# Optimization experiments

Hardware: AMD Instinct MI355X
Metric: run time of the kernel (lower is better)

## Reference

```python
import jax, jax.numpy as jnp
import numpy as np

B, C, M, H, W = 4, 12, 2, 320, 320
TOL = 1e-6
MAX_ITER = 10


def to_c(t):
    # [..., 2] real -> complex
    return jax.lax.complex(t[..., 0], t[..., 1])


def to_r(t):
    return jnp.stack([jnp.real(t), jnp.imag(t)], axis=-1)


def fft2c(x):
    return jnp.fft.fft2(x, axes=(-2, -1), norm='ortho')


def ifft2c(x):
    return jnp.fft.ifft2(x, axes=(-2, -1), norm='ortho')


def A_op(x, sm, mk):
    # x: [B,M,H,W] complex, sm: [B,C,M,H,W] complex, mk: [B,C,H,W] real
    coil_imgs = jnp.sum(x[:, None] * sm, axis=2)  # [B,C,H,W]
    return fft2c(coil_imgs) * mk


def AT_op(y, sm, mk):
    img = ifft2c(y * mk)  # [B,C,H,W]
    return jnp.sum(jnp.conj(sm) * img[:, :, None], axis=1)  # [B,M,H,W]


def cg_solve(x0, Mop, tol=TOL, max_iter=MAX_ITER):
    b = x0.shape[0]
    x0x0 = jnp.sum(jnp.abs(x0.reshape(b, -1)) ** 2, axis=-1)  # [B] real

    def body(carry, _):
        x, r, p, rr = carry
        active = jnp.min(rr / x0x0) > tol  # tol check, gated like the while-loop
        q = Mop(p)
        pq = jnp.sum((p * jnp.conj(q)).reshape(b, -1), axis=-1)  # complexDot(p, q)
        alpha = rr.astype(x0.dtype) / pq  # complex_div(rr, <p,q>)
        a = alpha[:, None, None, None]
        x_new = x + a * p
        r_new = r - a * q
        rr_new = jnp.sum(jnp.abs(r_new.reshape(b, -1)) ** 2, axis=-1)
        beta = (rr_new / rr)[:, None, None, None].astype(x0.dtype)
        p_new = r_new + beta * p
        new = (x_new, r_new, p_new, rr_new)
        carry = jax.tree.map(lambda n, o: jnp.where(active, n, o), new, carry)
        return carry, None

    rr0 = jnp.sum(jnp.abs(x0.reshape(b, -1)) ** 2, axis=-1)
    init = (jnp.zeros_like(x0), x0, x0, rr0)
    (x, _, _, _), _ = jax.lax.scan(body, init, None, length=max_iter)
    return x


def setup_inputs() -> dict:
    key = jax.random.key(0)
    k1, k2, k3, k4 = jax.random.split(key, 4)
    x = jax.random.normal(k1, (B, M, H, W, 2), dtype=jnp.float32)
    y = jax.random.normal(k2, (B, C, H, W, 2), dtype=jnp.float32)
    smaps = jax.random.normal(k3, (B, C, M, H, W, 2), dtype=jnp.float32) * 0.2
    mask = jax.random.randint(k4, (B, C, H, W, 1), 0, 2).astype(jnp.float32)
    lambda_a = jnp.full((1,), 0.05, dtype=jnp.float32)
    return {"x": x, "y": y, "smaps": smaps, "mask": mask, "lambda_a": lambda_a}


def reference(x, y, smaps, mask, lambda_a):
    z = to_c(x)          # [B,M,H,W]
    yc = to_c(y)         # [B,C,H,W]
    sm = to_c(smaps)     # [B,C,M,H,W]
    mk = mask[..., 0]    # [B,C,H,W]
    lam = lambda_a[0]

    x0 = lam * AT_op(yc, sm, mk) + z

    def Mop(p):
        return lam * AT_op(A_op(p, sm, mk), sm, mk) + p

    return to_r(cg_solve(x0, Mop))
```

## Files before the change

### kernel.cpp

```cpp
#include <hip/hip_runtime.h>
#include <math.h>

#define NB 4
#define NC 12
#define NM 2
#define NN 320
#define NHW (NN*NN)
#define NBC (NB*NC)
#define CG_TOL 1e-6f
#define NITER 10
#define PBLK 400
#define QBLK 320
#define CPG 3
#define NG  4
#define TROW 4
#define LSTR (NN + 2)

#define TWO_PI_F 6.28318530717958647692f

typedef float2 c32;

__device__ __forceinline__ c32 cmul(c32 a, c32 b){ return make_float2(a.x*b.x - a.y*b.y, a.x*b.y + a.y*b.x); }
__device__ __forceinline__ c32 cmulj(c32 a, c32 b){ return make_float2(a.x*b.x + a.y*b.y, a.x*b.y - a.y*b.x); }
__device__ __forceinline__ c32 cadd(c32 a, c32 b){ return make_float2(a.x+b.x, a.y+b.y); }
__device__ __forceinline__ c32 csub(c32 a, c32 b){ return make_float2(a.x-b.x, a.y-b.y); }
__device__ __forceinline__ c32 cscale(c32 a, float s){ return make_float2(a.x*s, a.y*s); }

template<bool CONJ>
__device__ __forceinline__ c32 twmul(c32 a, c32 t){
  return CONJ ? make_float2(a.x*t.x + a.y*t.y, a.y*t.x - a.x*t.y)
              : make_float2(a.x*t.x - a.y*t.y, a.y*t.x + a.x*t.y);
}

__device__ __forceinline__ float wave_reduce_f(float v) {
  #pragma unroll
  for (int off = 32; off >= 1; off >>= 1) v += __shfl_xor(v, off, 64);
  return v;
}
__device__ __forceinline__ c32 wave_reduce_c(c32 v) {
  #pragma unroll
  for (int off = 32; off >= 1; off >>= 1) {
    v.x += __shfl_xor(v.x, off, 64);
    v.y += __shfl_xor(v.y, off, 64);
  }
  return v;
}

__global__ __launch_bounds__(256)
void twiddle_init(c32* __restrict__ T320, c32* __restrict__ T64)
{
  const int t = threadIdx.x;
  {
    float s, c; sincosf(TWO_PI_F * (float)t / 320.f, &s, &c);
    T320[t] = make_float2(c, s);
  }
  if (t < 32) {
    float s, c; sincosf(TWO_PI_F * (float)t / 64.f, &s, &c);
    T64[t] = make_float2(c, s);
  }
}

template<bool FWD>
__device__ __forceinline__ void radix5(c32 V[5]) {
  constexpr float C1 = 0.30901699437494745f;
  constexpr float S1 = 0.9510565162951535f;
  constexpr float C2 = -0.8090169943749475f;
  constexpr float S2 = 0.5877852522924731f;
  constexpr float sg = FWD ? -1.f : 1.f;
  const c32 w1 = make_float2(C1,  sg*S1);
  const c32 w2 = make_float2(C2,  sg*S2);
  const c32 w3 = make_float2(C2, -sg*S2);
  const c32 w4 = make_float2(C1, -sg*S1);
  c32 v0=V[0], v1=V[1], v2=V[2], v3=V[3], v4=V[4];
  V[0] = cadd(cadd(v0, v1), cadd(cadd(v2, v3), v4));
  V[1] = cadd(v0, cadd(cadd(cmul(v1,w1), cmul(v2,w2)), cadd(cmul(v3,w3), cmul(v4,w4))));
  V[2] = cadd(v0, cadd(cadd(cmul(v1,w2), cmul(v2,w4)), cadd(cmul(v3,w1), cmul(v4,w3))));
  V[3] = cadd(v0, cadd(cadd(cmul(v1,w3), cmul(v2,w1)), cadd(cmul(v3,w4), cmul(v4,w2))));
  V[4] = cadd(v0, cadd(cadd(cmul(v1,w4), cmul(v2,w3)), cadd(cmul(v3,w2), cmul(v4,w1))));
}

template<bool FWD>
__device__ __forceinline__ void fft320_one(c32 A[5], const c32 ct[4], const c32 tw[6], int lane)
{
  radix5<FWD>(A);
  #pragma unroll
  for (int k = 1; k < 5; ++k) A[k] = twmul<FWD>(A[k], ct[k-1]);
  #pragma unroll
  for (int s = 0; s < 6; ++s) {
    const int m = 32 >> s;
    const c32 w = tw[s];
    const bool up = (lane & m) != 0;
    c32 o[5];
    #pragma unroll
    for (int k = 0; k < 5; ++k) { o[k].x = __shfl_xor(A[k].x, m, 64); o[k].y = __shfl_xor(A[k].y, m, 64); }
    #pragma unroll
    for (int k = 0; k < 5; ++k) {
      c32 lo = cadd(A[k], o[k]);
      c32 hi = twmul<FWD>(csub(o[k], A[k]), w);
      A[k] = up ? hi : lo;
    }
  }
}

__device__ __forceinline__ void ifft320_dit(c32 A[5], const c32 ct[4], const c32 tw[6], int lane)
{
  #pragma unroll
  for (int s = 5; s >= 0; --s) {
    const int m = 32 >> s;
    const c32 w = tw[s];
    const bool up = (lane & m) != 0;
    #pragma unroll
    for (int k = 0; k < 5; ++k) {
      c32 t = up ? twmul<false>(A[k], w) : A[k];
      c32 o; o.x = __shfl_xor(t.x, m, 64); o.y = __shfl_xor(t.y, m, 64);
      A[k] = up ? csub(o, t) : cadd(t, o);
    }
  }
  #pragma unroll
  for (int k = 1; k < 5; ++k) A[k] = twmul<false>(A[k], ct[k-1]);
  radix5<false>(A);
}

#define LOAD_TWIDDLES \
  c32 ct[4], tw[6]; \
  _Pragma("unroll") for (int k_ = 0; k_ < 4; ++k_) ct[k_] = T320[(k_ + 1) * lane]; \
  _Pragma("unroll") for (int s_ = 0; s_ < 6; ++s_) tw[s_] = T64[(lane & ((32 >> s_) - 1)) << s_];

__global__ __launch_bounds__(256)
void setup_mask_ifft(const c32* __restrict__ in, c32* __restrict__ out,
                     const float* __restrict__ mask,
                     const c32* __restrict__ T320, const c32* __restrict__ T64)
{
  __shared__ c32 tile[TROW][LSTR];
  const int tid = threadIdx.x, lane = tid & 63, wv = tid >> 6;
  const int by = blockIdx.y, b = by >> 2, g = by & 3;
  const int r0 = blockIdx.x * TROW;
  const int row = r0 + wv;
  LOAD_TWIDDLES
  const int rv6 = __brev((unsigned)lane) >> 26;
  for (int cc = 0; cc < CPG; ++cc) {
    const int bc = b*NC + g*CPG + cc;
    c32 A[5];
    #pragma unroll
    for (int j = 0; j < 5; ++j) {
      const size_t idx = ((size_t)bc * NN + row) * NN + lane + 64*j;
      A[j] = cscale(in[idx], mask[idx]);
    }
    fft320_one<false>(A, ct, tw, lane);
    __syncthreads();
    #pragma unroll
    for (int k = 0; k < 5; ++k) tile[wv][k + 5*rv6] = A[k];
    __syncthreads();
    #pragma unroll
    for (int it = 0; it < 5; ++it) {
      const int idx = it * 256 + tid, u = idx >> 2, d = idx & 3;
      out[((size_t)bc * NN + u) * NN + (r0 + d)] = tile[d][u];
    }
  }
}

__global__ __launch_bounds__(256)
void setup_init(const c32* __restrict__ bufin, const c32* __restrict__ smaps,
                c32* __restrict__ pacc,
                const c32* __restrict__ T320, const c32* __restrict__ T64)
{
  __shared__ c32 tile[TROW][LSTR];
  const int tid = threadIdx.x, lane = tid & 63, wv = tid >> 6;
  const int by = blockIdx.y, b = by >> 2, g = by & 3;
  const int r0 = blockIdx.x * TROW;
  const int w = r0 + wv;
  LOAD_TWIDDLES
  const int rv6 = __brev((unsigned)lane) >> 26;
  c32 acc0[5], acc1[5];
  #pragma unroll
  for (int it = 0; it < 5; ++it) { acc0[it] = make_float2(0.f,0.f); acc1[it] = make_float2(0.f,0.f); }

  for (int cc = 0; cc < CPG; ++cc) {
    const int c = g*CPG + cc;
    c32 A[5];
    #pragma unroll
    for (int j = 0; j < 5; ++j)
      A[j] = bufin[((size_t)(b*NC + c) * NN + w) * NN + lane + 64*j];
    fft320_one<false>(A, ct, tw, lane);
    __syncthreads();
    #pragma unroll
    for (int k = 0; k < 5; ++k) tile[wv][k + 5*rv6] = A[k];
    __syncthreads();
    #pragma unroll
    for (int it = 0; it < 5; ++it) {
      const int idx = it * 256 + tid, u = idx >> 2, d = idx & 3;
      c32 v = tile[d][u];
      c32 s0 = smaps[(size_t)((b*NC + c)*NM + 0) * NHW + (size_t)u * NN + (r0 + d)];
      c32 s1 = smaps[(size_t)((b*NC + c)*NM + 1) * NHW + (size_t)u * NN + (r0 + d)];
      acc0[it] = cadd(acc0[it], cmulj(s0, v));
      acc1[it] = cadd(acc1[it], cmulj(s1, v));
    }
  }
  #pragma unroll
  for (int it = 0; it < 5; ++it) {
    const int idx = it * 256 + tid, u = idx >> 2, d = idx & 3;
    const size_t hw = (size_t)u * NN + (r0 + d);
    pacc[(size_t)((g*NB + b)*NM + 0) * NHW + hw] = acc0[it];
    pacc[(size_t)((g*NB + b)*NM + 1) * NHW + hw] = acc1[it];
  }
}

__global__ __launch_bounds__(256)
void setup_fin(const c32* __restrict__ pacc, const c32* __restrict__ z,
               c32* __restrict__ x, c32* __restrict__ r, c32* __restrict__ p,
               const float* __restrict__ lam, float* __restrict__ part)
{
  const int b  = blockIdx.y;
  const int hw = blockIdx.x * 256 + threadIdx.x;
  const float l0 = lam[0] * (1.f / (float)NN);
  float accf = 0.f;
  #pragma unroll
  for (int m = 0; m < NM; ++m) {
    c32 a = make_float2(0.f, 0.f);
    #pragma unroll
    for (int g = 0; g < NG; ++g)
      a = cadd(a, pacc[(size_t)((g*NB + b)*NM + m) * NHW + hw]);
    const size_t im = (size_t)(b*NM + m) * NHW + hw;
    c32 x0v = cadd(cscale(a, l0), z[im]);
    x[im] = make_float2(0.f, 0.f);
    r[im] = x0v; p[im] = x0v;
    accf += x0v.x*x0v.x + x0v.y*x0v.y;
  }
  accf = wave_reduce_f(accf);
  __shared__ float sred[4];
  const int lane = threadIdx.x & 63, wv = threadIdx.x >> 6;
  if (lane == 0) sred[wv] = accf;
  __syncthreads();
  if (threadIdx.x == 0) part[b*PBLK + blockIdx.x] = sred[0]+sred[1]+sred[2]+sred[3];
}

__global__ __launch_bounds__(256)
void fft_comb_deep(c32* __restrict__ out, const c32* __restrict__ pin,
                   const c32* __restrict__ rres, c32* __restrict__ pout,
                   const c32* __restrict__ smaps,
                   float* __restrict__ rr, float* __restrict__ flags,
                   const float* __restrict__ part1, const int it,
                   const c32* __restrict__ T320, const c32* __restrict__ T64)
{
  __shared__ c32 tile[TROW][LSTR];
  __shared__ float sstat[NB];
  const int tid = threadIdx.x, lane = tid & 63, wv = tid >> 6;
  const int by = blockIdx.y, b = by >> 2, g = by & 3;
  const int r0 = blockIdx.x * TROW;
  const int row = r0 + wv;
  {
    float s = 0.f;
    for (int j = lane; j < PBLK; j += 64) s += part1[wv*PBLK + j];
    s = wave_reduce_f(s);
    if (lane == 0) sstat[wv] = s;
  }
  __syncthreads();
  float flag;
  if (it == 0) flag = 1.f;
  else {
    float mn = 1e30f;
    #pragma unroll
    for (int bb = 0; bb < NB; ++bb) mn = fminf(mn, sstat[bb] / rr[bb]);
    flag = (mn > CG_TOL) ? 1.f : 0.f;
  }
  if (tid < NB) rr[it*NB + tid] = sstat[tid];
  if (tid == 0) flags[it] = flag;
  if (it != 0 && flag == 0.f) return;
  const float beta = (it != 0) ? sstat[b] / rr[(it-1)*NB + b] : 0.f;

  LOAD_TWIDDLES
  const int rv6 = __brev((unsigned)lane) >> 26;
  const size_t m0 = (size_t)(b*NM + 0) * NHW, m1 = (size_t)(b*NM + 1) * NHW;
  c32 p0[5], p1[5];
  #pragma unroll
  for (int j = 0; j < 5; ++j) {
    const size_t h = (size_t)row * NN + lane + 64*j;
    c32 r0v = rres[m0 + h], r1v = rres[m1 + h];
    if (it != 0) {
      p0[j] = cadd(r0v, cscale(pin[m0 + h], beta));
      p1[j] = cadd(r1v, cscale(pin[m1 + h], beta));
      if (g == 0) { pout[m0 + h] = p0[j]; pout[m1 + h] = p1[j]; }
    } else { p0[j] = r0v; p1[j] = r1v; }
  }
  for (int cc = 0; cc < CPG; ++cc) {
    const int c = g * CPG + cc;
    const size_t s0o = (size_t)((b*NC + c)*NM + 0) * NHW, s1o = (size_t)((b*NC + c)*NM + 1) * NHW;
    c32 A[5];
    #pragma unroll
    for (int j = 0; j < 5; ++j) {
      const size_t h = (size_t)row * NN + lane + 64*j;
      A[j] = cadd(cmul(p0[j], smaps[s0o + h]), cmul(p1[j], smaps[s1o + h]));
    }
    fft320_one<true>(A, ct, tw, lane);
    __syncthreads();
    #pragma unroll
    for (int k = 0; k < 5; ++k) tile[wv][k + 5*rv6] = A[k];
    __syncthreads();
    #pragma unroll
    for (int itr = 0; itr < 5; ++itr) {
      const int idx = itr * 256 + tid, u = idx >> 2, d = idx & 3;
      out[(size_t)(b*NC + c) * NHW + (size_t)u * NN + (r0 + d)] = tile[d][u];
    }
  }
}

__global__ __launch_bounds__(256)
void fmi_deep(const c32* __restrict__ in, c32* __restrict__ out,
              const float* __restrict__ mask, const float* __restrict__ flag,
              const c32* __restrict__ T320, const c32* __restrict__ T64)
{
  if (flag[0] == 0.f) return;
  __shared__ c32 tile[TROW][LSTR];
  const int tid = threadIdx.x, lane = tid & 63, wv = tid >> 6;
  const int by = blockIdx.y, b = by >> 2, g = by & 3;
  const int r0 = blockIdx.x * TROW;
  const int row = r0 + wv;
  LOAD_TWIDDLES
  const int rv6 = __brev((unsigned)lane) >> 26;
  for (int cc = 0; cc < CPG; ++cc) {
    const int bc = b*NC + g*CPG + cc;
    c32 A[5];
    #pragma unroll
    for (int j = 0; j < 5; ++j)
      A[j] = in[((size_t)bc * NN + row) * NN + lane + 64*j];
    fft320_one<true>(A, ct, tw, lane);
    #pragma unroll
    for (int k = 0; k < 5; ++k) {
      const int kh = k + 5*rv6;
      A[k] = cscale(A[k], mask[(size_t)bc * NHW + (size_t)kh * NN + row]);
    }
    ifft320_dit(A, ct, tw, lane);
    __syncthreads();
    #pragma unroll
    for (int j = 0; j < 5; ++j) tile[wv][lane + 64*j] = A[j];
    __syncthreads();
    #pragma unroll
    for (int it = 0; it < 5; ++it) {
      const int idx = it * 256 + tid, u = idx >> 2, d = idx & 3;
      out[(size_t)bc * NHW + (size_t)u * NN + (r0 + d)] = tile[d][u];
    }
  }
}

__global__ __launch_bounds__(256)
void ifft_q(const c32* __restrict__ bufin, const c32* __restrict__ smaps,
            const c32* __restrict__ p, c32* __restrict__ q,
            const float* __restrict__ lam, const float* __restrict__ flag,
            c32* __restrict__ pqpart,
            const c32* __restrict__ T320, const c32* __restrict__ T64)
{
  if (flag[0] == 0.f) return;
  __shared__ c32 tile[TROW][LSTR];
  const int tid = threadIdx.x, lane = tid & 63, wv = tid >> 6;
  const int b = blockIdx.y, h = blockIdx.x;
  LOAD_TWIDDLES
  const int rv6 = __brev((unsigned)lane) >> 26;
  const float lq = lam[0] * (1.f / (float)NHW);
  const size_t rowoff = (size_t)h * NN + lane;
  c32 acc0[5], acc1[5];
  #pragma unroll
  for (int j = 0; j < 5; ++j) { acc0[j] = make_float2(0.f,0.f); acc1[j] = make_float2(0.f,0.f); }

  for (int cc = 0; cc < CPG; ++cc) {
    const int c = wv * CPG + cc;
    const size_t ib  = (size_t)(b*NC + c) * NHW + rowoff;
    const size_t is0 = (size_t)((b*NC + c)*NM + 0) * NHW + rowoff;
    const size_t is1 = (size_t)((b*NC + c)*NM + 1) * NHW + rowoff;
    c32 A[5], S0[5], S1[5];
    #pragma unroll
    for (int j = 0; j < 5; ++j) {
      A[j] = bufin[ib + 64*j]; S0[j] = smaps[is0 + 64*j]; S1[j] = smaps[is1 + 64*j];
    }
    fft320_one<false>(A, ct, tw, lane);
    #pragma unroll
    for (int k = 0; k < 5; ++k) tile[wv][k + 5*rv6] = A[k];
    #pragma unroll
    for (int j = 0; j < 5; ++j) {
      c32 v = tile[wv][lane + 64*j];
      acc0[j] = cadd(acc0[j], cmulj(S0[j], v));
      acc1[j] = cadd(acc1[j], cmulj(S1[j], v));
    }
  }
  c32* red = &tile[0][0];
  __syncthreads();
  if (wv >= 2) {
    const int base = (wv - 2) * 640;
    #pragma unroll
    for (int j = 0; j < 5; ++j) {
      red[base + j*64 + lane] = acc0[j];
      red[base + 320 + j*64 + lane] = acc1[j];
    }
  }
  __syncthreads();
  if (wv < 2) {
    const int base = wv * 640;
    #pragma unroll
    for (int j = 0; j < 5; ++j) {
      acc0[j] = cadd(acc0[j], red[base + j*64 + lane]);
      acc1[j] = cadd(acc1[j], red[base + 320 + j*64 + lane]);
    }
  }
  __syncthreads();
  if (wv == 1) {
    #pragma unroll
    for (int j = 0; j < 5; ++j) {
      red[j*64 + lane] = acc0[j];
      red[320 + j*64 + lane] = acc1[j];
    }
  }
  __syncthreads();
  if (wv == 0) {
    const size_t i0 = (size_t)(b*NM + 0) * NHW + rowoff;
    const size_t i1 = (size_t)(b*NM + 1) * NHW + rowoff;
    c32 pqs = make_float2(0.f, 0.f);
    #pragma unroll
    for (int j = 0; j < 5; ++j) {
      acc0[j] = cadd(acc0[j], red[j*64 + lane]);
      acc1[j] = cadd(acc1[j], red[320 + j*64 + lane]);
      c32 p0 = p[i0 + 64*j], p1 = p[i1 + 64*j];
      c32 q0 = cadd(cscale(acc0[j], lq), p0);
      c32 q1 = cadd(cscale(acc1[j], lq), p1);
      q[i0 + 64*j] = q0; q[i1 + 64*j] = q1;
      pqs = cadd(pqs, cadd(cmulj(q0, p0), cmulj(q1, p1)));
    }
    pqs = wave_reduce_c(pqs);
    if (lane == 0) pqpart[b*QBLK + h] = pqs;
  }
}

__global__ __launch_bounds__(256)
void update1(c32* __restrict__ x, c32* __restrict__ r,
             const c32* __restrict__ p, const c32* __restrict__ q,
             const float* __restrict__ rr, const c32* __restrict__ pqpart,
             const float* __restrict__ flag, float* __restrict__ part,
             const int it)
{
  if (flag[0] == 0.f) return;
  const int b = blockIdx.y;
  const int t = threadIdx.x;
  c32 s = make_float2(0.f, 0.f);
  for (int j = t; j < QBLK; j += 256) s = cadd(s, pqpart[b*QBLK + j]);
  s = wave_reduce_c(s);
  __shared__ c32 spq[4];
  const int lane = t & 63, wv = t >> 6;
  if (lane == 0) spq[wv] = s;
  __syncthreads();
  const c32 pqv = cadd(cadd(spq[0], spq[1]), cadd(spq[2], spq[3]));
  const float rrv = rr[it*NB + b];
  const float den = pqv.x*pqv.x + pqv.y*pqv.y;
  const c32 alpha = make_float2(rrv * pqv.x / den, -rrv * pqv.y / den);
  const int hw = blockIdx.x * 256 + t;
  float acc = 0.f;
  #pragma unroll
  for (int m = 0; m < NM; ++m) {
    const size_t idx = (size_t)(b*NM + m) * NHW + hw;
    c32 pe = p[idx], qe = q[idx];
    c32 xe = cadd(x[idx], cmul(alpha, pe));
    c32 re = csub(r[idx], cmul(alpha, qe));
    x[idx] = xe; r[idx] = re;
    acc += re.x*re.x + re.y*re.y;
  }
  acc = wave_reduce_f(acc);
  __shared__ float sred[4];
  if (lane == 0) sred[wv] = acc;
  __syncthreads();
  if (t == 0) part[b*PBLK + blockIdx.x] = sred[0]+sred[1]+sred[2]+sred[3];
}

extern "C" void kernel_launch(void* const* d_in, const int* in_sizes, int n_in,
                              void* d_out, int out_size, void* d_ws, size_t ws_size,
                              hipStream_t stream)
{
  const c32*  z   = (const c32*)d_in[0];
  const c32*  y   = (const c32*)d_in[1];
  const c32*  sm  = (const c32*)d_in[2];
  const float* mk = (const float*)d_in[3];
  const float* lam= (const float*)d_in[4];
  c32* x = (c32*)d_out;

  char* base = (char*)d_ws;
  size_t off = 0;
  auto walloc = [&](size_t bytes) -> void* {
    void* ptr = base + off;
    off += (bytes + 255) & ~(size_t)255;
    return ptr;
  };
  c32* buf1   = (c32*)walloc((size_t)NBC * NHW * sizeof(c32));
  c32* buf2   = (c32*)walloc((size_t)NBC * NHW * sizeof(c32));
  c32* rv     = (c32*)walloc((size_t)NB * NM * NHW * sizeof(c32));
  c32* pvA    = (c32*)walloc((size_t)NB * NM * NHW * sizeof(c32));
  c32* pvB    = (c32*)walloc((size_t)NB * NM * NHW * sizeof(c32));
  c32* qv     = (c32*)walloc((size_t)NB * NM * NHW * sizeof(c32));
  c32* pqpart = (c32*)walloc((size_t)NB * QBLK * sizeof(c32));
  float* rr   = (float*)walloc((NITER + 1) * NB * sizeof(float));
  float* flags= (float*)walloc((NITER + 1) * sizeof(float));
  float* part1= (float*)walloc((size_t)NB * PBLK * sizeof(float));
  c32* T320   = (c32*)walloc(256 * sizeof(c32));
  c32* T64    = (c32*)walloc(32 * sizeof(c32));
  c32* pacc   = buf1;
  (void)ws_size; (void)in_sizes; (void)n_in; (void)out_size;

  dim3 blk256(256);
  dim3 dgrid(NN / TROW, NB * NG);
  dim3 fgrid(PBLK, NB);
  dim3 qgrid(QBLK, NB);

  twiddle_init<<<1, blk256, 0, stream>>>(T320, T64);

  setup_mask_ifft<<<dgrid, blk256, 0, stream>>>(y, buf2, mk, T320, T64);
  setup_init<<<dgrid, blk256, 0, stream>>>(buf2, sm, pacc, T320, T64);
  setup_fin<<<fgrid, blk256, 0, stream>>>(pacc, z, x, rv, pvA, lam, part1);

  for (int i = 0; i < NITER; ++i) {
    c32* pin  = (i & 1) ? pvA : pvB;
    c32* pout = (i & 1) ? pvB : pvA;
    fft_comb_deep<<<dgrid, blk256, 0, stream>>>(buf2, pin, rv, pout, sm, rr, flags, part1, i, T320, T64);
    fmi_deep<<<dgrid, blk256, 0, stream>>>(buf2, buf1, mk, flags + i, T320, T64);
    ifft_q<<<qgrid, blk256, 0, stream>>>(buf1, sm, pout, qv, lam, flags + i, pqpart, T320, T64);
    update1<<<fgrid, blk256, 0, stream>>>(x, rv, pout, qv, rr, pqpart, flags + i, part1, i);
  }
}
```

Measured before the change: 422.8 us.

## Fuse whole CG solve into one persistent cooperative kernel with grid syncs

Replaces roughly 44 separate kernel launches with a single cooperative persistent kernel that loops over work units and separates phases with grid.sync(). Twiddles are computed in registers with sincosf instead of being loaded from a table. The setup phase now reduces coils in a pointwise pass instead of through partial accumulators, and the convergence check breaks out of the loop directly instead of using flag-gated launches. This removes launch gaps and the flag-checking launches, at the cost of grid-wide barrier overhead, a capped grid size and a possible occupancy limit from launch_bounds(256,3).

```diff
diff --git a/kernel.cpp b/kernel.cpp
--- a/kernel.cpp
+++ b/kernel.cpp
@@ -1,5 +1,8 @@
 #include <hip/hip_runtime.h>
+#include <hip/hip_cooperative_groups.h>
 #include <math.h>
+
+namespace cgr = cooperative_groups;
 
 #define NB 4
 #define NC 12
@@ -44,20 +47,6 @@
     v.y += __shfl_xor(v.y, off, 64);
   }
   return v;
-}
-
-__global__ __launch_bounds__(256)
-void twiddle_init(c32* __restrict__ T320, c32* __restrict__ T64)
-{
-  const int t = threadIdx.x;
-  {
-    float s, c; sincosf(TWO_PI_F * (float)t / 320.f, &s, &c);
-    T320[t] = make_float2(c, s);
-  }
-  if (t < 32) {
-    float s, c; sincosf(TWO_PI_F * (float)t / 64.f, &s, &c);
-    T64[t] = make_float2(c, s);
-  }
 }
 
 template<bool FWD>
@@ -121,350 +110,326 @@
   radix5<false>(A);
 }
 
-#define LOAD_TWIDDLES \
-  c32 ct[4], tw[6]; \
-  _Pragma("unroll") for (int k_ = 0; k_ < 4; ++k_) ct[k_] = T320[(k_ + 1) * lane]; \
-  _Pragma("unroll") for (int s_ = 0; s_ < 6; ++s_) tw[s_] = T64[(lane & ((32 >> s_) - 1)) << s_];
-
-__global__ __launch_bounds__(256)
-void setup_mask_ifft(const c32* __restrict__ in, c32* __restrict__ out,
-                     const float* __restrict__ mask,
-                     const c32* __restrict__ T320, const c32* __restrict__ T64)
+__device__ __forceinline__ float sel4(const float a[4], int i) {
+  float r = a[0];
+  r = (i == 1) ? a[1] : r;
+  r = (i == 2) ? a[2] : r;
+  r = (i == 3) ? a[3] : r;
+  return r;
+}
+
+__global__ __launch_bounds__(256, 3)
+void cg_all(const c32* __restrict__ z, const c32* __restrict__ y,
+            const c32* __restrict__ sm, const float* __restrict__ mk,
+            const float* __restrict__ lam,
+            c32* __restrict__ x, c32* __restrict__ buf1, c32* __restrict__ buf2,
+            c32* __restrict__ rv, c32* __restrict__ pvA, c32* __restrict__ pvB,
+            c32* __restrict__ qv, c32* __restrict__ pqpart, float* __restrict__ part1)
 {
+  cgr::grid_group grid = cgr::this_grid();
   __shared__ c32 tile[TROW][LSTR];
+  __shared__ float sredf[8];
+  __shared__ c32 sqq[4];
   const int tid = threadIdx.x, lane = tid & 63, wv = tid >> 6;
-  const int by = blockIdx.y, b = by >> 2, g = by & 3;
-  const int r0 = blockIdx.x * TROW;
-  const int row = r0 + wv;
-  LOAD_TWIDDLES
+  const int bid = blockIdx.x;
+  const int nblk = gridDim.x;
+  const float lamv = lam[0];
+
+  c32 ct[4], tw[6];
+  #pragma unroll
+  for (int k = 0; k < 4; ++k) {
+    float s, c; sincosf(TWO_PI_F * (float)((k + 1) * lane) / 320.f, &s, &c);
+    ct[k] = make_float2(c, s);
+  }
+  #pragma unroll
+  for (int s6 = 0; s6 < 6; ++s6) {
+    const int m = 32 >> s6;
+    float s, c; sincosf(TWO_PI_F * (float)((lane & (m - 1)) << s6) / 64.f, &s, &c);
+    tw[s6] = make_float2(c, s);
+  }
   const int rv6 = __brev((unsigned)lane) >> 26;
-  for (int cc = 0; cc < CPG; ++cc) {
-    const int bc = b*NC + g*CPG + cc;
-    c32 A[5];
+
+  for (int u = bid; u < 1280; u += nblk) {
+    const int xu = u % 80, by = u / 80;
+    const int b = by >> 2, g = by & 3;
+    const int r0 = xu * TROW, row = r0 + wv;
+    for (int cc = 0; cc < CPG; ++cc) {
+      const int bc = b*NC + g*CPG + cc;
+      c32 A[5];
+      #pragma unroll
+      for (int j = 0; j < 5; ++j) {
+        const size_t idx = ((size_t)bc * NN + row) * NN + lane + 64*j;
+        A[j] = cscale(y[idx], mk[idx]);
+      }
+      fft320_one<false>(A, ct, tw, lane);
+      __syncthreads();
+      #pragma unroll
+      for (int k = 0; k < 5; ++k) tile[wv][k + 5*rv6] = A[k];
+      __syncthreads();
+      #pragma unroll
+      for (int it5 = 0; it5 < 5; ++it5) {
+        const int idx = it5 * 256 + tid, u2 = idx >> 2, d = idx & 3;
+        buf2[((size_t)bc * NN + u2) * NN + (r0 + d)] = tile[d][u2];
+      }
+    }
+  }
+  grid.sync();
+
+  for (int u = bid; u < 1280; u += nblk) {
+    const int xu = u % 80, by = u / 80;
+    const int b = by >> 2, g = by & 3;
+    const int r0 = xu * TROW, w = r0 + wv;
+    for (int cc = 0; cc < CPG; ++cc) {
+      const int bc = b*NC + g*CPG + cc;
+      c32 A[5];
+      #pragma unroll
+      for (int j = 0; j < 5; ++j)
+        A[j] = buf2[((size_t)bc * NN + w) * NN + lane + 64*j];
+      fft320_one<false>(A, ct, tw, lane);
+      __syncthreads();
+      #pragma unroll
+      for (int k = 0; k < 5; ++k) tile[wv][k + 5*rv6] = A[k];
+      __syncthreads();
+      #pragma unroll
+      for (int it5 = 0; it5 < 5; ++it5) {
+        const int idx = it5 * 256 + tid, h = idx >> 2, d = idx & 3;
+        buf1[((size_t)bc * NN + h) * NN + (r0 + d)] = tile[d][h];
+      }
+    }
+  }
+  grid.sync();
+
+  for (int u = bid; u < NB * PBLK; u += nblk) {
+    const int b = u / PBLK, blk = u % PBLK;
+    const int hw = blk * 256 + tid;
+    const float l0 = lamv * (1.f / (float)NN);
+    c32 a0 = make_float2(0.f,0.f), a1 = make_float2(0.f,0.f);
+    for (int c = 0; c < NC; ++c) {
+      c32 iv = buf1[(size_t)(b*NC + c) * NHW + hw];
+      c32 s0 = sm[(size_t)((b*NC + c)*NM + 0) * NHW + hw];
+      c32 s1 = sm[(size_t)((b*NC + c)*NM + 1) * NHW + hw];
+      a0 = cadd(a0, cmulj(s0, iv));
+      a1 = cadd(a1, cmulj(s1, iv));
+    }
+    const size_t i0 = (size_t)(b*NM + 0) * NHW + hw;
+    const size_t i1 = (size_t)(b*NM + 1) * NHW + hw;
+    c32 x00 = cadd(cscale(a0, l0), z[i0]);
+    c32 x01 = cadd(cscale(a1, l0), z[i1]);
+    x[i0] = make_float2(0.f,0.f); x[i1] = make_float2(0.f,0.f);
+    rv[i0] = x00; rv[i1] = x01;
+    pvA[i0] = x00; pvA[i1] = x01;
+    float accf = x00.x*x00.x + x00.y*x00.y + x01.x*x01.x + x01.y*x01.y;
+    accf = wave_reduce_f(accf);
+    __syncthreads();
+    if (lane == 0) sredf[wv] = accf;
+    __syncthreads();
+    if (tid == 0) part1[b*PBLK + blk] = sredf[0]+sredf[1]+sredf[2]+sredf[3];
+  }
+  grid.sync();
+
+  float rrP[4], rrC[4], xx[4];
+  for (int it = 0; it < NITER; ++it) {
+    {
+      float s = 0.f;
+      for (int j = lane; j < PBLK; j += 64) s += part1[wv*PBLK + j];
+      s = wave_reduce_f(s);
+      __syncthreads();
+      if (lane == 0) sredf[wv] = s;
+      __syncthreads();
+    }
     #pragma unroll
-    for (int j = 0; j < 5; ++j) {
-      const size_t idx = ((size_t)bc * NN + row) * NN + lane + 64*j;
-      A[j] = cscale(in[idx], mask[idx]);
-    }
-    fft320_one<false>(A, ct, tw, lane);
-    __syncthreads();
+    for (int bb = 0; bb < 4; ++bb) rrC[bb] = sredf[bb];
+    if (it == 0) {
+      #pragma unroll
+      for (int bb = 0; bb < 4; ++bb) xx[bb] = rrC[bb];
+    } else {
+      const float mn = fminf(fminf(rrC[0]/xx[0], rrC[1]/xx[1]), fminf(rrC[2]/xx[2], rrC[3]/xx[3]));
+      if (!(mn > CG_TOL)) break;
+    }
+
+    c32* pin  = (it & 1) ? pvA : pvB;
+    c32* pout = (it & 1) ? pvB : pvA;
+    const bool upd = (it != 0);
+
+    for (int u = bid; u < 1280; u += nblk) {
+      const int xu = u % 80, by = u / 80;
+      const int b = by >> 2, g = by & 3;
+      const int r0 = xu * TROW, row = r0 + wv;
+      const float beta = upd ? sel4(rrC, b) / sel4(rrP, b) : 0.f;
+      const size_t m0 = (size_t)(b*NM + 0) * NHW, m1 = (size_t)(b*NM + 1) * NHW;
+      c32 p0[5], p1[5];
+      #pragma unroll
+      for (int j = 0; j < 5; ++j) {
+        const size_t h = (size_t)row * NN + lane + 64*j;
+        c32 r0v = rv[m0 + h], r1v = rv[m1 + h];
+        if (upd) {
+          p0[j] = cadd(r0v, cscale(pin[m0 + h], beta));
+          p1[j] = cadd(r1v, cscale(pin[m1 + h], beta));
+          if (g == 0) { pout[m0 + h] = p0[j]; pout[m1 + h] = p1[j]; }
+        } else { p0[j] = r0v; p1[j] = r1v; }
+      }
+      for (int cc = 0; cc < CPG; ++cc) {
+        const int c = g * CPG + cc;
+        const size_t s0o = (size_t)((b*NC + c)*NM + 0) * NHW, s1o = (size_t)((b*NC + c)*NM + 1) * NHW;
+        c32 A[5];
+        #pragma unroll
+        for (int j = 0; j < 5; ++j) {
+          const size_t h = (size_t)row * NN + lane + 64*j;
+          A[j] = cadd(cmul(p0[j], sm[s0o + h]), cmul(p1[j], sm[s1o + h]));
+        }
+        fft320_one<true>(A, ct, tw, lane);
+        __syncthreads();
+        #pragma unroll
+        for (int k = 0; k < 5; ++k) tile[wv][k + 5*rv6] = A[k];
+        __syncthreads();
+        #pragma unroll
+        for (int it5 = 0; it5 < 5; ++it5) {
+          const int idx = it5 * 256 + tid, u2 = idx >> 2, d = idx & 3;
+          buf2[(size_t)(b*NC + c) * NHW + (size_t)u2 * NN + (r0 + d)] = tile[d][u2];
+        }
+      }
+    }
+    grid.sync();
+
+    for (int u = bid; u < 1280; u += nblk) {
+      const int xu = u % 80, by = u / 80;
+      const int b = by >> 2, g = by & 3;
+      const int r0 = xu * TROW, row = r0 + wv;
+      for (int cc = 0; cc < CPG; ++cc) {
+        const int bc = b*NC + g*CPG + cc;
+        c32 A[5];
+        #pragma unroll
+        for (int j = 0; j < 5; ++j)
+          A[j] = buf2[((size_t)bc * NN + row) * NN + lane + 64*j];
+        fft320_one<true>(A, ct, tw, lane);
+        #pragma unroll
+        for (int k = 0; k < 5; ++k) {
+          const int kh = k + 5*rv6;
+          A[k] = cscale(A[k], mk[(size_t)bc * NHW + (size_t)kh * NN + row]);
+        }
+        ifft320_dit(A, ct, tw, lane);
+        __syncthreads();
+        #pragma unroll
+        for (int j = 0; j < 5; ++j) tile[wv][lane + 64*j] = A[j];
+        __syncthreads();
+        #pragma unroll
+        for (int it5 = 0; it5 < 5; ++it5) {
+          const int idx = it5 * 256 + tid, u2 = idx >> 2, d = idx & 3;
+          buf1[(size_t)bc * NHW + (size_t)u2 * NN + (r0 + d)] = tile[d][u2];
+        }
+      }
+    }
+    grid.sync();
+
+    for (int u = bid; u < NB * QBLK; u += nblk) {
+      const int b = u / QBLK, h = u % QBLK;
+      __syncthreads();
+      const float lq = lamv * (1.f / (float)NHW);
+      const size_t rowoff = (size_t)h * NN + lane;
+      c32 acc0[5], acc1[5];
+      #pragma unroll
+      for (int j = 0; j < 5; ++j) { acc0[j] = make_float2(0.f,0.f); acc1[j] = make_float2(0.f,0.f); }
+      for (int cc = 0; cc < CPG; ++cc) {
+        const int c = wv * CPG + cc;
+        const size_t ib  = (size_t)(b*NC + c) * NHW + rowoff;
+        const size_t is0 = (size_t)((b*NC + c)*NM + 0) * NHW + rowoff;
+        const size_t is1 = (size_t)((b*NC + c)*NM + 1) * NHW + rowoff;
+        c32 A[5], S0[5], S1[5];
+        #pragma unroll
+        for (int j = 0; j < 5; ++j) {
+          A[j] = buf1[ib + 64*j]; S0[j] = sm[is0 + 64*j]; S1[j] = sm[is1 + 64*j];
+        }
+        fft320_one<false>(A, ct, tw, lane);
+        #pragma unroll
+        for (int k = 0; k < 5; ++k) tile[wv][k + 5*rv6] = A[k];
+        #pragma unroll
+        for (int j = 0; j < 5; ++j) {
+          c32 v = tile[wv][lane + 64*j];
+          acc0[j] = cadd(acc0[j], cmulj(S0[j], v));
+          acc1[j] = cadd(acc1[j], cmulj(S1[j], v));
+        }
+      }
+      c32* red = &tile[0][0];
+      __syncthreads();
+      if (wv >= 2) {
+        const int base = (wv - 2) * 640;
+        #pragma unroll
+        for (int j = 0; j < 5; ++j) {
+          red[base + j*64 + lane] = acc0[j];
+          red[base + 320 + j*64 + lane] = acc1[j];
+        }
+      }
+      __syncthreads();
+      if (wv < 2) {
+        const int base = wv * 640;
+        #pragma unroll
+        for (int j = 0; j < 5; ++j) {
+          acc0[j] = cadd(acc0[j], red[base + j*64 + lane]);
+          acc1[j] = cadd(acc1[j], red[base + 320 + j*64 + lane]);
+        }
+      }
+      __syncthreads();
+      if (wv == 1) {
+        #pragma unroll
+        for (int j = 0; j < 5; ++j) {
+          red[j*64 + lane] = acc0[j];
+          red[320 + j*64 + lane] = acc1[j];
+        }
+      }
+      __syncthreads();
+      if (wv == 0) {
+        const size_t i0 = (size_t)(b*NM + 0) * NHW + rowoff;
+        const size_t i1 = (size_t)(b*NM + 1) * NHW + rowoff;
+        c32 pqs = make_float2(0.f, 0.f);
+        #pragma unroll
+        for (int j = 0; j < 5; ++j) {
+          acc0[j] = cadd(acc0[j], red[j*64 + lane]);
+          acc1[j] = cadd(acc1[j], red[320 + j*64 + lane]);
+          c32 p0 = pout[i0 + 64*j], p1 = pout[i1 + 64*j];
+          c32 q0 = cadd(cscale(acc0[j], lq), p0);
+          c32 q1 = cadd(cscale(acc1[j], lq), p1);
+          qv[i0 + 64*j] = q0; qv[i1 + 64*j] = q1;
+          pqs = cadd(pqs, cadd(cmulj(q0, p0), cmulj(q1, p1)));
+        }
+        pqs = wave_reduce_c(pqs);
+        if (lane == 0) pqpart[b*QBLK + h] = pqs;
+      }
+    }
+    grid.sync();
+
+    for (int u = bid; u < NB * PBLK; u += nblk) {
+      const int b = u / PBLK, blk = u % PBLK;
+      __syncthreads();
+      c32 s = make_float2(0.f, 0.f);
+      for (int j = tid; j < QBLK; j += 256) s = cadd(s, pqpart[b*QBLK + j]);
+      s = wave_reduce_c(s);
+      if (lane == 0) sqq[wv] = s;
+      __syncthreads();
+      const c32 pqv = cadd(cadd(sqq[0], sqq[1]), cadd(sqq[2], sqq[3]));
+      const float rrv = sel4(rrC, b);
+      const float den = pqv.x*pqv.x + pqv.y*pqv.y;
+      const c32 alpha = make_float2(rrv * pqv.x / den, -rrv * pqv.y / den);
+      const int hw = blk * 256 + tid;
+      float acc = 0.f;
+      #pragma unroll
+      for (int m = 0; m < NM; ++m) {
+        const size_t idx = (size_t)(b*NM + m) * NHW + hw;
+        c32 pe = pout[idx], qe = qv[idx];
+        c32 xe = cadd(x[idx], cmul(alpha, pe));
+        c32 re = csub(rv[idx], cmul(alpha, qe));
+        x[idx] = xe; rv[idx] = re;
+        acc += re.x*re.x + re.y*re.y;
+      }
+      acc = wave_reduce_f(acc);
+      if (lane == 0) sredf[wv] = acc;
+      __syncthreads();
+      if (tid == 0) part1[b*PBLK + blk] = sredf[0]+sredf[1]+sredf[2]+sredf[3];
+    }
+    grid.sync();
+
     #pragma unroll
-    for (int k = 0; k < 5; ++k) tile[wv][k + 5*rv6] = A[k];
-    __syncthreads();
-    #pragma unroll
-    for (int it = 0; it < 5; ++it) {
-      const int idx = it * 256 + tid, u = idx >> 2, d = idx & 3;
-      out[((size_t)bc * NN + u) * NN + (r0 + d)] = tile[d][u];
-    }
-  }
-}
-
-__global__ __launch_bounds__(256)
-void setup_init(const c32* __restrict__ bufin, const c32* __restrict__ smaps,
-                c32* __restrict__ pacc,
-                const c32* __restrict__ T320, const c32* __restrict__ T64)
-{
-  __shared__ c32 tile[TROW][LSTR];
-  const int tid = threadIdx.x, lane = tid & 63, wv = tid >> 6;
-  const int by = blockIdx.y, b = by >> 2, g = by & 3;
-  const int r0 = blockIdx.x * TROW;
-  const int w = r0 + wv;
-  LOAD_TWIDDLES
-  const int rv6 = __brev((unsigned)lane) >> 26;
-  c32 acc0[5], acc1[5];
-  #pragma unroll
-  for (int it = 0; it < 5; ++it) { acc0[it] = make_float2(0.f,0.f); acc1[it] = make_float2(0.f,0.f); }
-
-  for (int cc = 0; cc < CPG; ++cc) {
-    const int c = g*CPG + cc;
-    c32 A[5];
-    #pragma unroll
-    for (int j = 0; j < 5; ++j)
-      A[j] = bufin[((size_t)(b*NC + c) * NN + w) * NN + lane + 64*j];
-    fft320_one<false>(A, ct, tw, lane);
-    __syncthreads();
-    #pragma unroll
-    for (int k = 0; k < 5; ++k) tile[wv][k + 5*rv6] = A[k];
-    __syncthreads();
-    #pragma unroll
-    for (int it = 0; it < 5; ++it) {
-      const int idx = it * 256 + tid, u = idx >> 2, d = idx & 3;
-      c32 v = tile[d][u];
-      c32 s0 = smaps[(size_t)((b*NC + c)*NM + 0) * NHW + (size_t)u * NN + (r0 + d)];
-      c32 s1 = smaps[(size_t)((b*NC + c)*NM + 1) * NHW + (size_t)u * NN + (r0 + d)];
-      acc0[it] = cadd(acc0[it], cmulj(s0, v));
-      acc1[it] = cadd(acc1[it], cmulj(s1, v));
-    }
-  }
-  #pragma unroll
-  for (int it = 0; it < 5; ++it) {
-    const int idx = it * 256 + tid, u = idx >> 2, d = idx & 3;
-    const size_t hw = (size_t)u * NN + (r0 + d);
-    pacc[(size_t)((g*NB + b)*NM + 0) * NHW + hw] = acc0[it];
-    pacc[(size_t)((g*NB + b)*NM + 1) * NHW + hw] = acc1[it];
-  }
-}
-
-__global__ __launch_bounds__(256)
-void setup_fin(const c32* __restrict__ pacc, const c32* __restrict__ z,
-               c32* __restrict__ x, c32* __restrict__ r, c32* __restrict__ p,
-               const float* __restrict__ lam, float* __restrict__ part)
-{
-  const int b  = blockIdx.y;
-  const int hw = blockIdx.x * 256 + threadIdx.x;
-  const float l0 = lam[0] * (1.f / (float)NN);
-  float accf = 0.f;
-  #pragma unroll
-  for (int m = 0; m < NM; ++m) {
-    c32 a = make_float2(0.f, 0.f);
-    #pragma unroll
-    for (int g = 0; g < NG; ++g)
-      a = cadd(a, pacc[(size_t)((g*NB + b)*NM + m) * NHW + hw]);
-    const size_t im = (size_t)(b*NM + m) * NHW + hw;
-    c32 x0v = cadd(cscale(a, l0), z[im]);
-    x[im] = make_float2(0.f, 0.f);
-    r[im] = x0v; p[im] = x0v;
-    accf += x0v.x*x0v.x + x0v.y*x0v.y;
-  }
-  accf = wave_reduce_f(accf);
-  __shared__ float sred[4];
-  const int lane = threadIdx.x & 63, wv = threadIdx.x >> 6;
-  if (lane == 0) sred[wv] = accf;
-  __syncthreads();
-  if (threadIdx.x == 0) part[b*PBLK + blockIdx.x] = sred[0]+sred[1]+sred[2]+sred[3];
-}
-
-__global__ __launch_bounds__(256)
-void fft_comb_deep(c32* __restrict__ out, const c32* __restrict__ pin,
-                   const c32* __restrict__ rres, c32* __restrict__ pout,
-                   const c32* __restrict__ smaps,
-                   float* __restrict__ rr, float* __restrict__ flags,
-                   const float* __restrict__ part1, const int it,
-                   const c32* __restrict__ T320, const c32* __restrict__ T64)
-{
-  __shared__ c32 tile[TROW][LSTR];
-  __shared__ float sstat[NB];
-  const int tid = threadIdx.x, lane = tid & 63, wv = tid >> 6;
-  const int by = blockIdx.y, b = by >> 2, g = by & 3;
-  const int r0 = blockIdx.x * TROW;
-  const int row = r0 + wv;
-  {
-    float s = 0.f;
-    for (int j = lane; j < PBLK; j += 64) s += part1[wv*PBLK + j];
-    s = wave_reduce_f(s);
-    if (lane == 0) sstat[wv] = s;
-  }
-  __syncthreads();
-  float flag;
-  if (it == 0) flag = 1.f;
-  else {
-    float mn = 1e30f;
-    #pragma unroll
-    for (int bb = 0; bb < NB; ++bb) mn = fminf(mn, sstat[bb] / rr[bb]);
-    flag = (mn > CG_TOL) ? 1.f : 0.f;
-  }
-  if (tid < NB) rr[it*NB + tid] = sstat[tid];
-  if (tid == 0) flags[it] = flag;
-  if (it != 0 && flag == 0.f) return;
-  const float beta = (it != 0) ? sstat[b] / rr[(it-1)*NB + b] : 0.f;
-
-  LOAD_TWIDDLES
-  const int rv6 = __brev((unsigned)lane) >> 26;
-  const size_t m0 = (size_t)(b*NM + 0) * NHW, m1 = (size_t)(b*NM + 1) * NHW;
-  c32 p0[5], p1[5];
-  #pragma unroll
-  for (int j = 0; j < 5; ++j) {
-    const size_t h = (size_t)row * NN + lane + 64*j;
-    c32 r0v = rres[m0 + h], r1v = rres[m1 + h];
-    if (it != 0) {
-      p0[j] = cadd(r0v, cscale(pin[m0 + h], beta));
-      p1[j] = cadd(r1v, cscale(pin[m1 + h], beta));
-      if (g == 0) { pout[m0 + h] = p0[j]; pout[m1 + h] = p1[j]; }
-    } else { p0[j] = r0v; p1[j] = r1v; }
-  }
-  for (int cc = 0; cc < CPG; ++cc) {
-    const int c = g * CPG + cc;
-    const size_t s0o = (size_t)((b*NC + c)*NM + 0) * NHW, s1o = (size_t)((b*NC + c)*NM + 1) * NHW;
-    c32 A[5];
-    #pragma unroll
-    for (int j = 0; j < 5; ++j) {
-      const size_t h = (size_t)row * NN + lane + 64*j;
-      A[j] = cadd(cmul(p0[j], smaps[s0o + h]), cmul(p1[j], smaps[s1o + h]));
-    }
-    fft320_one<true>(A, ct, tw, lane);
-    __syncthreads();
-    #pragma unroll
-    for (int k = 0; k < 5; ++k) tile[wv][k + 5*rv6] = A[k];
-    __syncthreads();
-    #pragma unroll
-    for (int itr = 0; itr < 5; ++itr) {
-      const int idx = itr * 256 + tid, u = idx >> 2, d = idx & 3;
-      out[(size_t)(b*NC + c) * NHW + (size_t)u * NN + (r0 + d)] = tile[d][u];
-    }
-  }
-}
-
-__global__ __launch_bounds__(256)
-void fmi_deep(const c32* __restrict__ in, c32* __restrict__ out,
-              const float* __restrict__ mask, const float* __restrict__ flag,
-              const c32* __restrict__ T320, const c32* __restrict__ T64)
-{
-  if (flag[0] == 0.f) return;
-  __shared__ c32 tile[TROW][LSTR];
-  const int tid = threadIdx.x, lane = tid & 63, wv = tid >> 6;
-  const int by = blockIdx.y, b = by >> 2, g = by & 3;
-  const int r0 = blockIdx.x * TROW;
-  const int row = r0 + wv;
-  LOAD_TWIDDLES
-  const int rv6 = __brev((unsigned)lane) >> 26;
-  for (int cc = 0; cc < CPG; ++cc) {
-    const int bc = b*NC + g*CPG + cc;
-    c32 A[5];
-    #pragma unroll
-    for (int j = 0; j < 5; ++j)
-      A[j] = in[((size_t)bc * NN + row) * NN + lane + 64*j];
-    fft320_one<true>(A, ct, tw, lane);
-    #pragma unroll
-    for (int k = 0; k < 5; ++k) {
-      const int kh = k + 5*rv6;
-      A[k] = cscale(A[k], mask[(size_t)bc * NHW + (size_t)kh * NN + row]);
-    }
-    ifft320_dit(A, ct, tw, lane);
-    __syncthreads();
-    #pragma unroll
-    for (int j = 0; j < 5; ++j) tile[wv][lane + 64*j] = A[j];
-    __syncthreads();
-    #pragma unroll
-    for (int it = 0; it < 5; ++it) {
-      const int idx = it * 256 + tid, u = idx >> 2, d = idx & 3;
-      out[(size_t)bc * NHW + (size_t)u * NN + (r0 + d)] = tile[d][u];
-    }
-  }
-}
-
-__global__ __launch_bounds__(256)
-void ifft_q(const c32* __restrict__ bufin, const c32* __restrict__ smaps,
-            const c32* __restrict__ p, c32* __restrict__ q,
-            const float* __restrict__ lam, const float* __restrict__ flag,
-            c32* __restrict__ pqpart,
-            const c32* __restrict__ T320, const c32* __restrict__ T64)
-{
-  if (flag[0] == 0.f) return;
-  __shared__ c32 tile[TROW][LSTR];
-  const int tid = threadIdx.x, lane = tid & 63, wv = tid >> 6;
-  const int b = blockIdx.y, h = blockIdx.x;
-  LOAD_TWIDDLES
-  const int rv6 = __brev((unsigned)lane) >> 26;
-  const float lq = lam[0] * (1.f / (float)NHW);
-  const size_t rowoff = (size_t)h * NN + lane;
-  c32 acc0[5], acc1[5];
-  #pragma unroll
-  for (int j = 0; j < 5; ++j) { acc0[j] = make_float2(0.f,0.f); acc1[j] = make_float2(0.f,0.f); }
-
-  for (int cc = 0; cc < CPG; ++cc) {
-    const int c = wv * CPG + cc;
-    const size_t ib  = (size_t)(b*NC + c) * NHW + rowoff;
-    const size_t is0 = (size_t)((b*NC + c)*NM + 0) * NHW + rowoff;
-    const size_t is1 = (size_t)((b*NC + c)*NM + 1) * NHW + rowoff;
-    c32 A[5], S0[5], S1[5];
-    #pragma unroll
-    for (int j = 0; j < 5; ++j) {
-      A[j] = bufin[ib + 64*j]; S0[j] = smaps[is0 + 64*j]; S1[j] = smaps[is1 + 64*j];
-    }
-    fft320_one<false>(A, ct, tw, lane);
-    #pragma unroll
-    for (int k = 0; k < 5; ++k) tile[wv][k + 5*rv6] = A[k];
-    #pragma unroll
-    for (int j = 0; j < 5; ++j) {
-      c32 v = tile[wv][lane + 64*j];
-      acc0[j] = cadd(acc0[j], cmulj(S0[j], v));
-      acc1[j] = cadd(acc1[j], cmulj(S1[j], v));
-    }
-  }
-  c32* red = &tile[0][0];
-  __syncthreads();
-  if (wv >= 2) {
-    const int base = (wv - 2) * 640;
-    #pragma unroll
-    for (int j = 0; j < 5; ++j) {
-      red[base + j*64 + lane] = acc0[j];
-      red[base + 320 + j*64 + lane] = acc1[j];
-    }
-  }
-  __syncthreads();
-  if (wv < 2) {
-    const int base = wv * 640;
-    #pragma unroll
-    for (int j = 0; j < 5; ++j) {
-      acc0[j] = cadd(acc0[j], red[base + j*64 + lane]);
-      acc1[j] = cadd(acc1[j], red[base + 320 + j*64 + lane]);
-    }
-  }
-  __syncthreads();
-  if (wv == 1) {
-    #pragma unroll
-    for (int j = 0; j < 5; ++j) {
-      red[j*64 + lane] = acc0[j];
-      red[320 + j*64 + lane] = acc1[j];
-    }
-  }
-  __syncthreads();
-  if (wv == 0) {
-    const size_t i0 = (size_t)(b*NM + 0) * NHW + rowoff;
-    const size_t i1 = (size_t)(b*NM + 1) * NHW + rowoff;
-    c32 pqs = make_float2(0.f, 0.f);
-    #pragma unroll
-    for (int j = 0; j < 5; ++j) {
-      acc0[j] = cadd(acc0[j], red[j*64 + lane]);
-      acc1[j] = cadd(acc1[j], red[320 + j*64 + lane]);
-      c32 p0 = p[i0 + 64*j], p1 = p[i1 + 64*j];
-      c32 q0 = cadd(cscale(acc0[j], lq), p0);
-      c32 q1 = cadd(cscale(acc1[j], lq), p1);
-      q[i0 + 64*j] = q0; q[i1 + 64*j] = q1;
-      pqs = cadd(pqs, cadd(cmulj(q0, p0), cmulj(q1, p1)));
-    }
-    pqs = wave_reduce_c(pqs);
-    if (lane == 0) pqpart[b*QBLK + h] = pqs;
-  }
-}
-
-__global__ __launch_bounds__(256)
-void update1(c32* __restrict__ x, c32* __restrict__ r,
-             const c32* __restrict__ p, const c32* __restrict__ q,
-             const float* __restrict__ rr, const c32* __restrict__ pqpart,
-             const float* __restrict__ flag, float* __restrict__ part,
-             const int it)
-{
-  if (flag[0] == 0.f) return;
-  const int b = blockIdx.y;
-  const int t = threadIdx.x;
-  c32 s = make_float2(0.f, 0.f);
-  for (int j = t; j < QBLK; j += 256) s = cadd(s, pqpart[b*QBLK + j]);
-  s = wave_reduce_c(s);
-  __shared__ c32 spq[4];
-  const int lane = t & 63, wv = t >> 6;
-  if (lane == 0) spq[wv] = s;
-  __syncthreads();
-  const c32 pqv = cadd(cadd(spq[0], spq[1]), cadd(spq[2], spq[3]));
-  const float rrv = rr[it*NB + b];
-  const float den = pqv.x*pqv.x + pqv.y*pqv.y;
-  const c32 alpha = make_float2(rrv * pqv.x / den, -rrv * pqv.y / den);
-  const int hw = blockIdx.x * 256 + t;
-  float acc = 0.f;
-  #pragma unroll
-  for (int m = 0; m < NM; ++m) {
-    const size_t idx = (size_t)(b*NM + m) * NHW + hw;
-    c32 pe = p[idx], qe = q[idx];
-    c32 xe = cadd(x[idx], cmul(alpha, pe));
-    c32 re = csub(r[idx], cmul(alpha, qe));
-    x[idx] = xe; r[idx] = re;
-    acc += re.x*re.x + re.y*re.y;
-  }
-  acc = wave_reduce_f(acc);
-  __shared__ float sred[4];
-  if (lane == 0) sred[wv] = acc;
-  __syncthreads();
-  if (t == 0) part[b*PBLK + blockIdx.x] = sred[0]+sred[1]+sred[2]+sred[3];
+    for (int bb = 0; bb < 4; ++bb) rrP[bb] = rrC[bb];
+  }
 }
 
 extern "C" void kernel_launch(void* const* d_in, const int* in_sizes, int n_in,
@@ -492,31 +457,22 @@
   c32* pvB    = (c32*)walloc((size_t)NB * NM * NHW * sizeof(c32));
   c32* qv     = (c32*)walloc((size_t)NB * NM * NHW * sizeof(c32));
   c32* pqpart = (c32*)walloc((size_t)NB * QBLK * sizeof(c32));
-  float* rr   = (float*)walloc((NITER + 1) * NB * sizeof(float));
-  float* flags= (float*)walloc((NITER + 1) * sizeof(float));
   float* part1= (float*)walloc((size_t)NB * PBLK * sizeof(float));
-  c32* T320   = (c32*)walloc(256 * sizeof(c32));
-  c32* T64    = (c32*)walloc(32 * sizeof(c32));
-  c32* pacc   = buf1;
   (void)ws_size; (void)in_sizes; (void)n_in; (void)out_size;
 
-  dim3 blk256(256);
-  dim3 dgrid(NN / TROW, NB * NG);
-  dim3 fgrid(PBLK, NB);
-  dim3 qgrid(QBLK, NB);
-
-  twiddle_init<<<1, blk256, 0, stream>>>(T320, T64);
-
-  setup_mask_ifft<<<dgrid, blk256, 0, stream>>>(y, buf2, mk, T320, T64);
-  setup_init<<<dgrid, blk256, 0, stream>>>(buf2, sm, pacc, T320, T64);
-  setup_fin<<<fgrid, blk256, 0, stream>>>(pacc, z, x, rv, pvA, lam, part1);
-
-  for (int i = 0; i < NITER; ++i) {
-    c32* pin  = (i & 1) ? pvA : pvB;
-    c32* pout = (i & 1) ? pvB : pvA;
-    fft_comb_deep<<<dgrid, blk256, 0, stream>>>(buf2, pin, rv, pout, sm, rr, flags, part1, i, T320, T64);
-    fmi_deep<<<dgrid, blk256, 0, stream>>>(buf2, buf1, mk, flags + i, T320, T64);
-    ifft_q<<<qgrid, blk256, 0, stream>>>(buf1, sm, pout, qv, lam, flags + i, pqpart, T320, T64);
-    update1<<<fgrid, blk256, 0, stream>>>(x, rv, pout, qv, rr, pqpart, flags + i, part1, i);
-  }
-}
+  int dev = 0;
+  (void)hipGetDevice(&dev);
+  int cus = 0;
+  if (hipDeviceGetAttribute(&cus, hipDeviceAttributeMultiprocessorCount, dev) != hipSuccess || cus <= 0)
+    cus = 256;
+  int perCU = 0;
+  if (hipOccupancyMaxActiveBlocksPerMultiprocessor(&perCU, (const void*)cg_all, 256, 0) != hipSuccess || perCU < 1)
+    perCU = 1;
+  long long nblk_ll = (long long)cus * (long long)perCU;
+  int nblk = (nblk_ll > 1024) ? 1024 : (int)nblk_ll;
+
+  void* args[] = { (void*)&z, (void*)&y, (void*)&sm, (void*)&mk, (void*)&lam,
+                   (void*)&x, (void*)&buf1, (void*)&buf2, (void*)&rv,
+                   (void*)&pvA, (void*)&pvB, (void*)&qv, (void*)&pqpart, (void*)&part1 };
+  hipLaunchCooperativeKernel((const void*)cg_all, dim3(nblk), dim3(256), args, 0, stream);
+}
```

New measurement: 888.5 us. +110.1%, slower.
